# Kernel tuning notes

Measured on AMD Instinct MI355X. Metric: run time of the kernel, lower is better.

Reference implementation:

```python
import jax, jax.numpy as jnp
import numpy as np

B, G, D = 256, 64, 20          # batch, genes per term, subsystem output dim
T3, T2, T1, T0 = 2048, 512, 128, 1  # terms per stratum, deepest first
FAN = 4                        # children per internal term (root gets all T1)
EPS = 1e-5                     # BatchNorm1d eps


def setup_inputs() -> dict:
    key = jax.random.key(0)
    ks = jax.random.split(key, 32)
    def genes(k, T):
        # binary gene perturbation states (column 3 of go_gene_strata_state)
        return (jax.random.uniform(k, (B, T, G)) < 0.5).astype(jnp.float32)
    def lin(kw, kb, T, din):
        # nn.init.uniform_(w, -0.001, 0.001) per DCellSubsystem
        W = jax.random.uniform(kw, (T, din, D), minval=-0.001, maxval=0.001)
        b = jax.random.uniform(kb, (T, D), minval=-0.001, maxval=0.001)
        return W, b
    in3, in2, in1, in0 = G, FAN * D + G, FAN * D + G, T1 * D + G
    W3, b3 = lin(ks[0], ks[1], T3, in3)
    W2, b2 = lin(ks[2], ks[3], T2, in2)
    W1, b1 = lin(ks[4], ks[5], T1, in1)
    W0, b0 = lin(ks[6], ks[7], T0, in0)
    ones = lambda T: jnp.ones((T, D), jnp.float32)
    zeros = lambda T: jnp.zeros((T, D), jnp.float32)
    hw0 = jax.random.normal(ks[8], (T0, D, 1)) * 0.1
    hb0 = jnp.zeros((T0, 1), jnp.float32)
    return {
        'genes3': genes(ks[9], T3), 'genes2': genes(ks[10], T2),
        'genes1': genes(ks[11], T1), 'genes0': genes(ks[12], T0),
        'W3': W3, 'b3': b3, 'g3': ones(T3), 'be3': zeros(T3),
        'W2': W2, 'b2': b2, 'g2': ones(T2), 'be2': zeros(T2),
        'W1': W1, 'b1': b1, 'g1': ones(T1), 'be1': zeros(T1),
        'W0': W0, 'b0': b0, 'g0': ones(T0), 'be0': zeros(T0),
        'hw0': hw0, 'hb0': hb0,
    }


def _subsystem(x, W, b, g, be):
    # Linear -> BatchNorm1d (training mode, batch stats over axis 0) -> Tanh
    z = jnp.einsum('bti,tio->bto', x, W) + b          # [B, T, D]
    mu = jnp.mean(z, axis=0)
    var = jnp.var(z, axis=0)                           # biased, as in torch BN
    zn = (z - mu) * jax.lax.rsqrt(var + EPS)
    return jnp.tanh(zn * g + be)


def reference(genes3, genes2, genes1, genes0,
              W3, b3, g3, be3, W2, b2, g2, be2,
              W1, b1, g1, be1, W0, b0, g0, be0, hw0, hb0):
    # stratum 3 (leaves): input is gene states only
    h3 = _subsystem(genes3, W3, b3, g3, be3)           # [B, T3, D]
    # stratum 2: concat FAN contiguous children + own gene states
    x2 = jnp.concatenate([h3.reshape(B, T2, FAN * D), genes2], axis=-1)
    h2 = _subsystem(x2, W2, b2, g2, be2)               # [B, T2, D]
    x1 = jnp.concatenate([h2.reshape(B, T1, FAN * D), genes1], axis=-1)
    h1 = _subsystem(x1, W1, b1, g1, be1)               # [B, T1, D]
    # root: all T1 children + root gene states
    x0 = jnp.concatenate([h1.reshape(B, T0, T1 * D), genes0], axis=-1)
    h0 = _subsystem(x0, W0, b0, g0, be0)               # [B, 1, D]
    pred = jnp.einsum('bto,toc->btc', h0, hw0) + hb0   # root linear head
    return pred.reshape(B, 1)
```

## Files before the change

### kernel.cpp

```cpp
#include <hip/hip_runtime.h>
#include <hip/hip_fp16.h>


#define DEV static __device__ __forceinline__

constexpr int B_  = 256, G_ = 64, D_ = 20;
constexpr int T3_ = 2048, T2_ = 512, T1_ = 128;
constexpr float EPS_ = 1e-5f;

typedef unsigned char u8;
typedef unsigned long long u64;

constexpr size_t OFF_H2B = 0;
constexpr size_t SZ_H2 = (size_t)T2_ * B_ * D_ * 2;
constexpr size_t OFF_H1B = OFF_H2B + SZ_H2;
constexpr size_t SZ_H1 = (size_t)T1_ * B_ * D_ * 2;
constexpr size_t OFF_Z0B = OFF_H1B + SZ_H1;

typedef _Float16 half8_t __attribute__((ext_vector_type(8)));
typedef float f32x4 __attribute__((ext_vector_type(4)));

DEV half8_t as_h8(uint4 u) {
    union { uint4 u4; half8_t h; } c; c.u4 = u; return c.h;
}

DEV half8_t bits8_to_h8(uint byte) {
    uint4 r;
    r.x = ((byte & 1u)        | ((byte & 2u)   << 15)) * 0x3C00u;
    r.y = (((byte >> 2) & 1u) | ((byte & 8u)   << 13)) * 0x3C00u;
    r.z = (((byte >> 4) & 1u) | ((byte & 32u)  << 11)) * 0x3C00u;
    r.w = (((byte >> 6) & 1u) | ((byte & 128u) << 9))  * 0x3C00u;
    return as_h8(r);
}

DEV float fast_tanh(float x) {
    float e = __expf(2.0f * x);
    return fmaf(-2.0f, __builtin_amdgcn_rcpf(e + 1.0f), 1.0f);
}

__global__ __launch_bounds__(256, 2) void k_gemm32(
        const float* __restrict__ genes3, const float* __restrict__ genes2,
        const float* __restrict__ W3, const float* __restrict__ g3,
        const float* __restrict__ be3,
        const float* __restrict__ W2, const float* __restrict__ g2,
        const float* __restrict__ be2, __half* __restrict__ h2out) {
    constexpr int STRB3 = 72, STRB2 = 200;
    __shared__ __align__(16) __half h3loc[4 * B_ * D_ + 16];
    __shared__ __align__(16) __half WT3[2][32 * STRB3];
    __shared__ __align__(16) __half WT2[32 * STRB2];
    __shared__ u64 gmask[5][B_];
    __shared__ float sredb[2][4][16], qredb[2][4][16];
    __shared__ float gv3[4 * D_], bev3[4 * D_], gv2[D_], bev2[D_];

    const int t = blockIdx.x, tid = threadIdx.x;
    const int w = tid >> 6, lane = tid & 63;

    const int rb = w * 64;
#pragma unroll
    for (int s = 0; s < 5; ++s) {
        const float* gp = (s < 4)
            ? genes3 + ((size_t)rb * T3_ + 4 * t + s) * G_ + lane
            : genes2 + ((size_t)rb * T2_ + t) * G_ + lane;
        const size_t str = (size_t)(s < 4 ? T3_ : T2_) * G_;
        u64 my = 0;
#pragma unroll
        for (int r0 = 0; r0 < 64; r0 += 16) {
            float x[16];
#pragma unroll
            for (int r = 0; r < 16; ++r) x[r] = gp[(size_t)(r0 + r) * str];
#pragma unroll
            for (int r = 0; r < 16; ++r) {
                u64 m = __ballot(x[r] != 0.0f);
                if (lane == r0 + r) my = m;
            }
        }
        gmask[s][rb + lane] = my;
    }

    {
        uint* WTu = (uint*)WT2;
        for (int j = tid; j < 32 * STRB2 / 2; j += 256) WTu[j] = 0;
        if (tid < 16) h3loc[4 * B_ * D_ + tid] = __half(0.0f);
    }
    __syncthreads();

    if (tid < 4 * D_) {
        gv3[tid] = g3[(size_t)(4 * t) * D_ + tid];
        bev3[tid] = be3[(size_t)(4 * t) * D_ + tid];
    } else if (tid < 5 * D_) {
        gv2[tid - 4 * D_] = g2[(size_t)t * D_ + (tid - 4 * D_)];
        bev2[tid - 4 * D_] = be2[(size_t)t * D_ + (tid - 4 * D_)];
    }
    {
        const float* Wt = W2 + (size_t)t * (144 * D_);
        for (int j = tid; j < 144 * D_; j += 256) {
            int k_orig = j / D_, o = j - k_orig * D_;
            int k_lds;
            if (k_orig < 4 * D_) {
                int c = k_orig / D_;
                k_lds = c * 32 + (k_orig - c * D_);
            } else {
                k_lds = 4 * 32 + (k_orig - 4 * D_);
            }
            WT2[o * STRB2 + k_lds] = __float2half(Wt[j]);
        }
        const float* W3t = W3 + (size_t)(4 * t) * (G_ * D_);
#pragma unroll
        for (int i = 0; i < 5; ++i) {
            int j = tid + i * 256;
            int k = j / D_, o = j - k * D_;
            WT3[0][o * STRB3 + k] = __float2half(W3t[j]);
        }
    }
    __syncthreads();

    const int quad = lane >> 4, l15 = lane & 15;
    const int nt = w >> 1, mhalf = w & 1;
    const int ocol = nt * 16 + l15;
    const int brow_base = mhalf * 128;
    const int shq = quad * 8;
    const int oc = ocol < D_ ? ocol : D_ - 1;

#pragma unroll
    for (int c = 0; c < 4; ++c) {
        float wreg[5];
        if (c < 3) {
            const float* W3n = W3 + (size_t)(4 * t + c + 1) * (G_ * D_);
#pragma unroll
            for (int i = 0; i < 5; ++i) wreg[i] = W3n[tid + i * 256];
        }
        const __half* WTc = WT3[c & 1];
        half8_t Bf0 = as_h8(*(const uint4*)(WTc + ocol * STRB3 + quad * 8));
        half8_t Bf1 = as_h8(*(const uint4*)(WTc + ocol * STRB3 + 32 + quad * 8));

        f32x4 acc[8];
#pragma unroll
        for (int mt = 0; mt < 8; ++mt) acc[mt] = (f32x4){0.f, 0.f, 0.f, 0.f};
#pragma unroll
        for (int mt = 0; mt < 8; ++mt) {
            const int bA = brow_base + mt * 16 + l15;
            const u64 gm = gmask[c][bA];
            acc[mt] = __builtin_amdgcn_mfma_f32_16x16x32_f16(
                bits8_to_h8(((uint)gm >> shq) & 0xFFu), Bf0, acc[mt], 0, 0, 0);
            acc[mt] = __builtin_amdgcn_mfma_f32_16x16x32_f16(
                bits8_to_h8(((uint)(gm >> 32) >> shq) & 0xFFu), Bf1, acc[mt], 0, 0, 0);
        }

        if (c < 3) {
#pragma unroll
            for (int i = 0; i < 5; ++i) {
                int j = tid + i * 256;
                int k = j / D_, o = j - k * D_;
                WT3[(c + 1) & 1][o * STRB3 + k] = __float2half(wreg[i]);
            }
        }

        float s = 0.f, q = 0.f;
#pragma unroll
        for (int mt = 0; mt < 8; ++mt)
#pragma unroll
            for (int r = 0; r < 4; ++r) {
                float z = acc[mt][r];
                s += z; q += z * z;
            }
        s += __shfl_xor(s, 16, 64); q += __shfl_xor(q, 16, 64);
        s += __shfl_xor(s, 32, 64); q += __shfl_xor(q, 32, 64);
        if (lane < 16) { sredb[c & 1][w][lane] = s; qredb[c & 1][w][lane] = q; }
        __syncthreads();
        const float S = sredb[c & 1][2 * nt][l15] + sredb[c & 1][2 * nt + 1][l15];
        const float Q = qredb[c & 1][2 * nt][l15] + qredb[c & 1][2 * nt + 1][l15];
        const float mu  = S * (1.0f / B_);
        const float var = fmaxf(Q * (1.0f / B_) - mu * mu, 0.0f);
        const float rstd = rsqrtf(var + EPS_);
        const float A = rstd * gv3[c * D_ + oc];
        const float C = bev3[c * D_ + oc] - mu * A;
        if (ocol < D_) {
#pragma unroll
            for (int mt = 0; mt < 8; ++mt)
#pragma unroll
                for (int r = 0; r < 4; ++r) {
                    float h = fast_tanh(fmaf(A, acc[mt][r], C));
                    int b = brow_base + mt * 16 + quad * 4 + r;
                    h3loc[(size_t)(c * B_ + b) * D_ + ocol] = __float2half(h);
                }
        }
    }
    __syncthreads();

    half8_t Bf[6];
#pragma unroll
    for (int ks = 0; ks < 6; ++ks)
        Bf[ks] = as_h8(*(const uint4*)(WT2 + ocol * STRB2 + ks * 32 + quad * 8));

    f32x4 acc[8];
#pragma unroll
    for (int mt = 0; mt < 8; ++mt) acc[mt] = (f32x4){0.f, 0.f, 0.f, 0.f};
#pragma unroll
    for (int mt = 0; mt < 8; ++mt) {
        const int bA = brow_base + mt * 16 + l15;
        const u64 gm = gmask[4][bA];
#pragma unroll
        for (int c = 0; c < 4; ++c) {
            const __half* ap = h3loc + (size_t)(c * B_ + bA) * D_ + quad * 8;
            uint2 u0 = *(const uint2*)(ap);
            uint2 u1 = *(const uint2*)(ap + 4);
            acc[mt] = __builtin_amdgcn_mfma_f32_16x16x32_f16(
                as_h8(make_uint4(u0.x, u0.y, u1.x, u1.y)), Bf[c], acc[mt], 0, 0, 0);
        }
        acc[mt] = __builtin_amdgcn_mfma_f32_16x16x32_f16(
            bits8_to_h8(((uint)gm >> shq) & 0xFFu), Bf[4], acc[mt], 0, 0, 0);
        acc[mt] = __builtin_amdgcn_mfma_f32_16x16x32_f16(
            bits8_to_h8(((uint)(gm >> 32) >> shq) & 0xFFu), Bf[5], acc[mt], 0, 0, 0);
    }

    float s = 0.f, q = 0.f;
#pragma unroll
    for (int mt = 0; mt < 8; ++mt)
#pragma unroll
        for (int r = 0; r < 4; ++r) {
            float z = acc[mt][r];
            s += z; q += z * z;
        }
    s += __shfl_xor(s, 16, 64); q += __shfl_xor(q, 16, 64);
    s += __shfl_xor(s, 32, 64); q += __shfl_xor(q, 32, 64);
    if (lane < 16) { sredb[0][w][lane] = s; qredb[0][w][lane] = q; }
    __syncthreads();
    const float S = sredb[0][2 * nt][l15] + sredb[0][2 * nt + 1][l15];
    const float Q = qredb[0][2 * nt][l15] + qredb[0][2 * nt + 1][l15];
    const float mu  = S * (1.0f / B_);
    const float var = fmaxf(Q * (1.0f / B_) - mu * mu, 0.0f);
    const float rstd = rsqrtf(var + EPS_);
    const float A = rstd * gv2[oc];
    const float C = bev2[oc] - mu * A;

    __half* ebuf = WT2;
    if (ocol < D_) {
#pragma unroll
        for (int mt = 0; mt < 8; ++mt)
#pragma unroll
            for (int r = 0; r < 4; ++r) {
                float h = fast_tanh(fmaf(A, acc[mt][r], C));
                int b = brow_base + mt * 16 + quad * 4 + r;
                ebuf[b * D_ + ocol] = __float2half(h);
            }
    }
    __syncthreads();
    const uint4* src4 = (const uint4*)ebuf;
    uint4* dst4 = (uint4*)(h2out + (size_t)t * (B_ * D_));
    for (int j = tid; j < (B_ * D_) / 8; j += 256) dst4[j] = src4[j];
}

template <int T, int NCHILD>
__global__ __launch_bounds__(256, 4) void k_gemm(const __half* __restrict__ hsrc,
                                                 const float* __restrict__ genes,
                                                 const float* __restrict__ W,
                                                 const float* __restrict__ g,
                                                 const float* __restrict__ be,
                                                 __half* __restrict__ hout) {
    constexpr int K_IN = NCHILD * 20 + 64;
    constexpr int NK = NCHILD + 2;
    constexpr int STRB = NCHILD ? 200 : 72;
    constexpr int LDSH = (32 * STRB > B_ * D_) ? 32 * STRB : B_ * D_;
    __shared__ __align__(16) __half WT[LDSH];
    __shared__ float gv[D_], bev[D_];
    __shared__ float sred[4][16], qred[4][16];
    __shared__ u64 gmask[B_];

    const int t = blockIdx.x, tid = threadIdx.x;
    const int w = tid >> 6, lane = tid & 63;

    {
        const float* gp = genes + ((size_t)(w * 64) * T + t) * G_ + lane;
        u64 my = 0;
#pragma unroll
        for (int r0 = 0; r0 < 64; r0 += 16) {
            float x[16];
#pragma unroll
            for (int r = 0; r < 16; ++r)
                x[r] = gp[(size_t)(r0 + r) * (T * G_)];
#pragma unroll
            for (int r = 0; r < 16; ++r) {
                u64 m = __ballot(x[r] != 0.0f);
                if (lane == r0 + r) my = m;
            }
        }
        gmask[w * 64 + lane] = my;
    }

    if (NCHILD) {
        uint* WTu = (uint*)WT;
        for (int j = tid; j < 32 * STRB / 2; j += 256) WTu[j] = 0;
        __syncthreads();
    }
    if (tid < D_) { gv[tid] = g[t * D_ + tid]; bev[tid] = be[t * D_ + tid]; }
    const float* Wt = W + (size_t)t * (K_IN * D_);
    for (int j = tid; j < K_IN * D_; j += 256) {
        int k_orig = j / D_, o = j - k_orig * D_;
        int k_lds;
        if (NCHILD && k_orig < NCHILD * D_) {
            int c = k_orig / D_;
            k_lds = c * 32 + (k_orig - c * D_);
        } else {
            k_lds = NCHILD * 32 + (k_orig - NCHILD * D_);
        }
        WT[o * STRB + k_lds] = __float2half(Wt[j]);
    }
    __syncthreads();

    const int quad = lane >> 4, l15 = lane & 15;
    const int nt = w >> 1, mhalf = w & 1;
    const int ocol = nt * 16 + l15;
    const int brow_base = mhalf * 128;
    const int shq = quad * 8;

    half8_t Bf[NK];
#pragma unroll
    for (int ks = 0; ks < NK; ++ks)
        Bf[ks] = as_h8(*(const uint4*)(WT + ocol * STRB + ks * 32 + quad * 8));

    f32x4 acc[8];
#pragma unroll
    for (int mt = 0; mt < 8; ++mt) acc[mt] = (f32x4){0.f, 0.f, 0.f, 0.f};

#pragma unroll
    for (int mt = 0; mt < 8; ++mt) {
        const int bA = brow_base + mt * 16 + l15;
        const u64 gm = gmask[bA];
#pragma unroll
        for (int c = 0; c < NCHILD; ++c) {
            const __half* ap = hsrc + ((size_t)(NCHILD * t + c) * B_ + bA) * D_ + quad * 8;
            uint2 u0 = *(const uint2*)(ap);
            uint2 u1 = *(const uint2*)(ap + 4);
            acc[mt] = __builtin_amdgcn_mfma_f32_16x16x32_f16(
                as_h8(make_uint4(u0.x, u0.y, u1.x, u1.y)), Bf[c], acc[mt], 0, 0, 0);
        }
        acc[mt] = __builtin_amdgcn_mfma_f32_16x16x32_f16(
            bits8_to_h8(((uint)gm >> shq) & 0xFFu), Bf[NCHILD], acc[mt], 0, 0, 0);
        acc[mt] = __builtin_amdgcn_mfma_f32_16x16x32_f16(
            bits8_to_h8(((uint)(gm >> 32) >> shq) & 0xFFu), Bf[NCHILD + 1], acc[mt], 0, 0, 0);
    }

    float s = 0.f, q = 0.f;
#pragma unroll
    for (int mt = 0; mt < 8; ++mt)
#pragma unroll
        for (int r = 0; r < 4; ++r) {
            float z = acc[mt][r];
            s += z; q += z * z;
        }
    s += __shfl_xor(s, 16, 64); q += __shfl_xor(q, 16, 64);
    s += __shfl_xor(s, 32, 64); q += __shfl_xor(q, 32, 64);
    if (lane < 16) { sred[w][lane] = s; qred[w][lane] = q; }
    __syncthreads();
    const float S = sred[2 * nt][l15] + sred[2 * nt + 1][l15];
    const float Q = qred[2 * nt][l15] + qred[2 * nt + 1][l15];
    const float mu  = S * (1.0f / B_);
    const float var = fmaxf(Q * (1.0f / B_) - mu * mu, 0.0f);
    const float rstd = rsqrtf(var + EPS_);
    const int oc = ocol < D_ ? ocol : D_ - 1;
    const float A = rstd * gv[oc];
    const float C = bev[oc] - mu * A;

    if (ocol < D_) {
#pragma unroll
        for (int mt = 0; mt < 8; ++mt)
#pragma unroll
            for (int r = 0; r < 4; ++r) {
                float h = fast_tanh(fmaf(A, acc[mt][r], C));
                int b = brow_base + mt * 16 + quad * 4 + r;
                WT[b * D_ + ocol] = __float2half(h);
            }
    }
    __syncthreads();
    const uint4* src4 = (const uint4*)WT;
    uint4* dst4 = (uint4*)(hout + (size_t)t * (B_ * D_));
    for (int j = tid; j < (B_ * D_) / 8; j += 256) dst4[j] = src4[j];
}

__global__ __launch_bounds__(256, 4) void k_stage0a(const __half* __restrict__ h1,
                                                    const float* __restrict__ genes0,
                                                    const float* __restrict__ W0,
                                                    float* __restrict__ z0p) {
    const int b = blockIdx.x >> 2, s = blockIdx.x & 3, tid = threadIdx.x;
    const int kbase = 640 * s;
    float acc[D_] = {};
#pragma unroll
    for (int j = 0; j < 3; ++j) {
        int kl = tid + 256 * j;
        if (kl < 640) {
            int k = kbase + kl;
            int tt = k / D_, o = k - tt * D_;
            float xk = __half2float(h1[((size_t)tt * B_ + b) * D_ + o]);
            const float4* w = (const float4*)(W0 + (size_t)k * D_);
#pragma unroll
            for (int v = 0; v < D_ / 4; ++v) {
                float4 f = w[v];
                acc[4 * v + 0] = fmaf(xk, f.x, acc[4 * v + 0]);
                acc[4 * v + 1] = fmaf(xk, f.y, acc[4 * v + 1]);
                acc[4 * v + 2] = fmaf(xk, f.z, acc[4 * v + 2]);
                acc[4 * v + 3] = fmaf(xk, f.w, acc[4 * v + 3]);
            }
        }
    }
    if (s == 3 && tid < G_) {
        float xk = genes0[(size_t)b * G_ + tid];
        const float4* w = (const float4*)(W0 + (size_t)(T1_ * D_ + tid) * D_);
#pragma unroll
        for (int v = 0; v < D_ / 4; ++v) {
            float4 f = w[v];
            acc[4 * v + 0] = fmaf(xk, f.x, acc[4 * v + 0]);
            acc[4 * v + 1] = fmaf(xk, f.y, acc[4 * v + 1]);
            acc[4 * v + 2] = fmaf(xk, f.z, acc[4 * v + 2]);
            acc[4 * v + 3] = fmaf(xk, f.w, acc[4 * v + 3]);
        }
    }
    __shared__ float sred[4][D_];
    const int lane = tid & 63, wave = tid >> 6;
#pragma unroll
    for (int off = 32; off; off >>= 1)
#pragma unroll
        for (int o = 0; o < D_; ++o) acc[o] += __shfl_xor(acc[o], off, 64);
    if (lane == 0)
#pragma unroll
        for (int o = 0; o < D_; ++o) sred[wave][o] = acc[o];
    __syncthreads();
    if (tid < D_)
        z0p[((size_t)b * 4 + s) * D_ + tid] =
            sred[0][tid] + sred[1][tid] + sred[2][tid] + sred[3][tid];
}

__global__ __launch_bounds__(256) void k_stage0b(const float* __restrict__ z0p,
                                                 const float* __restrict__ g0,
                                                 const float* __restrict__ be0,
                                                 const float* __restrict__ hw0,
                                                 const float* __restrict__ hb0,
                                                 float* __restrict__ out) {
    const int tid = threadIdx.x;
    float acc[D_] = {};
#pragma unroll
    for (int s = 0; s < 4; ++s) {
        const float4* zp = (const float4*)(z0p + ((size_t)tid * 4 + s) * D_);
#pragma unroll
        for (int v = 0; v < D_ / 4; ++v) {
            float4 f = zp[v];
            acc[4 * v + 0] += f.x; acc[4 * v + 1] += f.y;
            acc[4 * v + 2] += f.z; acc[4 * v + 3] += f.w;
        }
    }
    __shared__ float sred[4][D_], qred[4][D_], Avec[D_], Cvec[D_], hwv[D_ + 1];
    const int lane = tid & 63, wave = tid >> 6;
    float s[D_], q[D_];
#pragma unroll
    for (int o = 0; o < D_; ++o) { s[o] = acc[o]; q[o] = acc[o] * acc[o]; }
#pragma unroll
    for (int off = 32; off; off >>= 1) {
#pragma unroll
        for (int o = 0; o < D_; ++o) {
            s[o] += __shfl_xor(s[o], off, 64);
            q[o] += __shfl_xor(q[o], off, 64);
        }
    }
    if (lane == 0) {
#pragma unroll
        for (int o = 0; o < D_; ++o) { sred[wave][o] = s[o]; qred[wave][o] = q[o]; }
    }
    __syncthreads();
    if (tid < D_) {
        float S = sred[0][tid] + sred[1][tid] + sred[2][tid] + sred[3][tid];
        float Q = qred[0][tid] + qred[1][tid] + qred[2][tid] + qred[3][tid];
        float mu  = S * (1.0f / B_);
        float var = fmaxf(Q * (1.0f / B_) - mu * mu, 0.0f);
        float rstd = rsqrtf(var + EPS_);
        float A = rstd * g0[tid];
        Avec[tid] = A;
        Cvec[tid] = be0[tid] - mu * A;
        hwv[tid] = hw0[tid];
    }
    if (tid == 0) hwv[D_] = hb0[0];
    __syncthreads();
    float pred = hwv[D_];
#pragma unroll
    for (int o = 0; o < D_; ++o) {
        float h = fast_tanh(fmaf(acc[o], Avec[o], Cvec[o]));
        pred = fmaf(h, hwv[o], pred);
    }
    out[tid] = pred;
}

extern "C" void kernel_launch(void* const* d_in, const int* in_sizes, int n_in,
                              void* d_out, int out_size, void* d_ws, size_t ws_size,
                              hipStream_t stream) {
    const float* genes3 = (const float*)d_in[0];
    const float* genes2 = (const float*)d_in[1];
    const float* genes1 = (const float*)d_in[2];
    const float* genes0 = (const float*)d_in[3];
    const float* W3  = (const float*)d_in[4];
    const float* g3  = (const float*)d_in[6];
    const float* be3 = (const float*)d_in[7];
    const float* W2  = (const float*)d_in[8];
    const float* g2  = (const float*)d_in[10];
    const float* be2 = (const float*)d_in[11];
    const float* W1  = (const float*)d_in[12];
    const float* g1  = (const float*)d_in[14];
    const float* be1 = (const float*)d_in[15];
    const float* W0  = (const float*)d_in[16];
    const float* g0  = (const float*)d_in[18];
    const float* be0 = (const float*)d_in[19];
    const float* hw0 = (const float*)d_in[20];
    const float* hb0 = (const float*)d_in[21];

    char* wsb = (char*)d_ws;
    __half* h2  = (__half*)(wsb + OFF_H2B);
    __half* h1  = (__half*)(wsb + OFF_H1B);
    float*  z0p = (float*)(wsb + OFF_Z0B);

    k_gemm32<<<T2_, 256, 0, stream>>>(genes3, genes2, W3, g3, be3,
                                      W2, g2, be2, h2);
    k_gemm<T1_, 4><<<T1_, 256, 0, stream>>>(h2, genes1, W1, g1, be1, h1);
    k_stage0a<<<B_ * 4, 256, 0, stream>>>(h1, genes0, W0, z0p);
    k_stage0b<<<1, 256, 0, stream>>>(z0p, g0, be0, hw0, hb0, (float*)d_out);
}
```

Measured before the change: 318.7 us.

## Prefetch next gene-mask section during MFMA and batch weight staging loads

The up-front gene bitmask construction for all five sections is replaced by building only section 0 first. Each following section's genes are loaded and ballot-packed inside the per-child loop, split around the two halves of the MFMA work, so global latency overlaps compute. Weight staging for W2, W3 and the generic stratum kernel now issues all global loads into registers before converting and scattering into LDS, which lets loads pipeline. The cost is higher register pressure (32-float buffers plus staging arrays), which could hurt occupancy under launch_bounds(256,2).

```diff
diff --git a/kernel.cpp b/kernel.cpp
--- a/kernel.cpp
+++ b/kernel.cpp
@@ -54,33 +54,33 @@
 
     const int t = blockIdx.x, tid = threadIdx.x;
     const int w = tid >> 6, lane = tid & 63;
-
     const int rb = w * 64;
-#pragma unroll
-    for (int s = 0; s < 5; ++s) {
-        const float* gp = (s < 4)
-            ? genes3 + ((size_t)rb * T3_ + 4 * t + s) * G_ + lane
-            : genes2 + ((size_t)rb * T2_ + t) * G_ + lane;
-        const size_t str = (size_t)(s < 4 ? T3_ : T2_) * G_;
-        u64 my = 0;
-#pragma unroll
-        for (int r0 = 0; r0 < 64; r0 += 16) {
-            float x[16];
-#pragma unroll
-            for (int r = 0; r < 16; ++r) x[r] = gp[(size_t)(r0 + r) * str];
-#pragma unroll
-            for (int r = 0; r < 16; ++r) {
-                u64 m = __ballot(x[r] != 0.0f);
-                if (lane == r0 + r) my = m;
-            }
-        }
-        gmask[s][rb + lane] = my;
-    }
+    const size_t str3 = (size_t)T3_ * G_;
 
     {
-        uint* WTu = (uint*)WT2;
-        for (int j = tid; j < 32 * STRB2 / 2; j += 256) WTu[j] = 0;
-        if (tid < 16) h3loc[4 * B_ * D_ + tid] = __half(0.0f);
+        const float* gp0 = genes3 + ((size_t)rb * T3_ + 4 * t) * G_ + lane;
+        float x[32];
+#pragma unroll
+        for (int r = 0; r < 32; ++r) x[r] = gp0[(size_t)r * str3];
+        {
+            uint* WTu = (uint*)WT2;
+            for (int j = tid; j < 32 * STRB2 / 2; j += 256) WTu[j] = 0;
+            if (tid < 16) h3loc[4 * B_ * D_ + tid] = __half(0.0f);
+        }
+        u64 my0 = 0;
+#pragma unroll
+        for (int r = 0; r < 32; ++r) {
+            u64 m = __ballot(x[r] != 0.0f);
+            if (lane == r) my0 = m;
+        }
+#pragma unroll
+        for (int r = 0; r < 32; ++r) x[r] = gp0[(size_t)(32 + r) * str3];
+#pragma unroll
+        for (int r = 0; r < 32; ++r) {
+            u64 m = __ballot(x[r] != 0.0f);
+            if (lane == 32 + r) my0 = m;
+        }
+        gmask[0][rb + lane] = my0;
     }
     __syncthreads();
 
@@ -92,24 +92,38 @@
         bev2[tid - 4 * D_] = be2[(size_t)t * D_ + (tid - 4 * D_)];
     }
     {
+        constexpr int NW2 = (144 * D_ + 255) / 256;
         const float* Wt = W2 + (size_t)t * (144 * D_);
-        for (int j = tid; j < 144 * D_; j += 256) {
-            int k_orig = j / D_, o = j - k_orig * D_;
-            int k_lds;
-            if (k_orig < 4 * D_) {
-                int c = k_orig / D_;
-                k_lds = c * 32 + (k_orig - c * D_);
-            } else {
-                k_lds = 4 * 32 + (k_orig - 4 * D_);
-            }
-            WT2[o * STRB2 + k_lds] = __float2half(Wt[j]);
+        float wst[NW2];
+#pragma unroll
+        for (int i = 0; i < NW2; ++i) {
+            int j = tid + i * 256;
+            wst[i] = (j < 144 * D_) ? Wt[j] : 0.0f;
         }
         const float* W3t = W3 + (size_t)(4 * t) * (G_ * D_);
+        float w3st[5];
+#pragma unroll
+        for (int i = 0; i < 5; ++i) w3st[i] = W3t[tid + i * 256];
+#pragma unroll
+        for (int i = 0; i < NW2; ++i) {
+            int j = tid + i * 256;
+            if (j < 144 * D_) {
+                int k_orig = j / D_, o = j - k_orig * D_;
+                int k_lds;
+                if (k_orig < 4 * D_) {
+                    int c = k_orig / D_;
+                    k_lds = c * 32 + (k_orig - c * D_);
+                } else {
+                    k_lds = 4 * 32 + (k_orig - 4 * D_);
+                }
+                WT2[o * STRB2 + k_lds] = __float2half(wst[i]);
+            }
+        }
 #pragma unroll
         for (int i = 0; i < 5; ++i) {
             int j = tid + i * 256;
             int k = j / D_, o = j - k * D_;
-            WT3[0][o * STRB3 + k] = __float2half(W3t[j]);
+            WT3[0][o * STRB3 + k] = __float2half(w3st[i]);
         }
     }
     __syncthreads();
@@ -123,6 +137,16 @@
 
 #pragma unroll
     for (int c = 0; c < 4; ++c) {
+        const int sec = c + 1;
+        const float* gpn = (sec < 4)
+            ? genes3 + ((size_t)rb * T3_ + 4 * t + sec) * G_ + lane
+            : genes2 + ((size_t)rb * T2_ + t) * G_ + lane;
+        const size_t strn = (sec < 4) ? str3 : (size_t)T2_ * G_;
+
+        float x[32];
+#pragma unroll
+        for (int r = 0; r < 32; ++r) x[r] = gpn[(size_t)r * strn];
+
         float wreg[5];
         if (c < 3) {
             const float* W3n = W3 + (size_t)(4 * t + c + 1) * (G_ * D_);
@@ -136,8 +160,9 @@
         f32x4 acc[8];
 #pragma unroll
         for (int mt = 0; mt < 8; ++mt) acc[mt] = (f32x4){0.f, 0.f, 0.f, 0.f};
-#pragma unroll
-        for (int mt = 0; mt < 8; ++mt) {
+
+#pragma unroll
+        for (int mt = 0; mt < 4; ++mt) {
             const int bA = brow_base + mt * 16 + l15;
             const u64 gm = gmask[c][bA];
             acc[mt] = __builtin_amdgcn_mfma_f32_16x16x32_f16(
@@ -145,6 +170,32 @@
             acc[mt] = __builtin_amdgcn_mfma_f32_16x16x32_f16(
                 bits8_to_h8(((uint)(gm >> 32) >> shq) & 0xFFu), Bf1, acc[mt], 0, 0, 0);
         }
+
+        u64 myn = 0;
+#pragma unroll
+        for (int r = 0; r < 32; ++r) {
+            u64 m = __ballot(x[r] != 0.0f);
+            if (lane == r) myn = m;
+        }
+#pragma unroll
+        for (int r = 0; r < 32; ++r) x[r] = gpn[(size_t)(32 + r) * strn];
+
+#pragma unroll
+        for (int mt = 4; mt < 8; ++mt) {
+            const int bA = brow_base + mt * 16 + l15;
+            const u64 gm = gmask[c][bA];
+            acc[mt] = __builtin_amdgcn_mfma_f32_16x16x32_f16(
+                bits8_to_h8(((uint)gm >> shq) & 0xFFu), Bf0, acc[mt], 0, 0, 0);
+            acc[mt] = __builtin_amdgcn_mfma_f32_16x16x32_f16(
+                bits8_to_h8(((uint)(gm >> 32) >> shq) & 0xFFu), Bf1, acc[mt], 0, 0, 0);
+        }
+
+#pragma unroll
+        for (int r = 0; r < 32; ++r) {
+            u64 m = __ballot(x[r] != 0.0f);
+            if (lane == 32 + r) myn = m;
+        }
+        gmask[sec][rb + lane] = myn;
 
         if (c < 3) {
 #pragma unroll
@@ -293,17 +344,30 @@
         __syncthreads();
     }
     if (tid < D_) { gv[tid] = g[t * D_ + tid]; bev[tid] = be[t * D_ + tid]; }
-    const float* Wt = W + (size_t)t * (K_IN * D_);
-    for (int j = tid; j < K_IN * D_; j += 256) {
-        int k_orig = j / D_, o = j - k_orig * D_;
-        int k_lds;
-        if (NCHILD && k_orig < NCHILD * D_) {
-            int c = k_orig / D_;
-            k_lds = c * 32 + (k_orig - c * D_);
-        } else {
-            k_lds = NCHILD * 32 + (k_orig - NCHILD * D_);
-        }
-        WT[o * STRB + k_lds] = __float2half(Wt[j]);
+    {
+        constexpr int NST = (K_IN * D_ + 255) / 256;
+        const float* Wt = W + (size_t)t * (K_IN * D_);
+        float wst[NST];
+#pragma unroll
+        for (int i = 0; i < NST; ++i) {
+            int j = tid + i * 256;
+            wst[i] = (j < K_IN * D_) ? Wt[j] : 0.0f;
+        }
+#pragma unroll
+        for (int i = 0; i < NST; ++i) {
+            int j = tid + i * 256;
+            if (j < K_IN * D_) {
+                int k_orig = j / D_, o = j - k_orig * D_;
+                int k_lds;
+                if (NCHILD && k_orig < NCHILD * D_) {
+                    int c = k_orig / D_;
+                    k_lds = c * 32 + (k_orig - c * D_);
+                } else {
+                    k_lds = NCHILD * 32 + (k_orig - NCHILD * D_);
+                }
+                WT[o * STRB + k_lds] = __float2half(wst[i]);
+            }
+        }
     }
     __syncthreads();
 
```

Result: faster. 306.0 us (-4.0%).

## Pre-pack gene states into transposed bitmasks with a coalesced pass

Applied to the files above, without the earlier changes.

Adds a kernel that reads the float gene arrays row-contiguously, ballots each row into a 64-bit mask and writes the masks transposed per term. The GEMM kernels then load one u64 per thread instead of doing strided per-batch gene reads. The weight staging loops are also split so all global loads are issued into registers before the LDS conversion stores. The cost is an extra launch, extra workspace, and a round trip of the mask data through global memory.

```diff
diff --git a/kernel.cpp b/kernel.cpp
--- a/kernel.cpp
+++ b/kernel.cpp
@@ -11,7 +11,13 @@
 typedef unsigned char u8;
 typedef unsigned long long u64;
 
-constexpr size_t OFF_H2B = 0;
+constexpr size_t OFF_GTB3 = 0;
+constexpr size_t SZ_GTB3 = (size_t)T3_ * B_ * 8;
+constexpr size_t OFF_GTB2 = OFF_GTB3 + SZ_GTB3;
+constexpr size_t SZ_GTB2 = (size_t)T2_ * B_ * 8;
+constexpr size_t OFF_GTB1 = OFF_GTB2 + SZ_GTB2;
+constexpr size_t SZ_GTB1 = (size_t)T1_ * B_ * 8;
+constexpr size_t OFF_H2B = OFF_GTB1 + SZ_GTB1;
 constexpr size_t SZ_H2 = (size_t)T2_ * B_ * D_ * 2;
 constexpr size_t OFF_H1B = OFF_H2B + SZ_H2;
 constexpr size_t SZ_H1 = (size_t)T1_ * B_ * D_ * 2;
@@ -38,8 +44,44 @@
     return fmaf(-2.0f, __builtin_amdgcn_rcpf(e + 1.0f), 1.0f);
 }
 
+__global__ __launch_bounds__(256, 8) void k_pack_all(
+        const float* __restrict__ g3s, const float* __restrict__ g2s,
+        const float* __restrict__ g1s,
+        u64* __restrict__ d3, u64* __restrict__ d2, u64* __restrict__ d1) {
+    constexpr int R3 = B_ * T3_;
+    constexpr int R2 = B_ * T2_;
+    const int lane = threadIdx.x & 63;
+    int R0 = (blockIdx.x * 4 + (threadIdx.x >> 6)) * 8;
+    const float* src; u64* dst; int shift;
+    if (R0 < R3)            { src = g3s; dst = d3; shift = 11; }
+    else if (R0 < R3 + R2)  { R0 -= R3; src = g2s; dst = d2; shift = 9; }
+    else                    { R0 -= R3 + R2; src = g1s; dst = d1; shift = 7; }
+
+    const float* p = src + (size_t)R0 * G_ + lane;
+    float x[8];
+#pragma unroll
+    for (int r = 0; r < 8; ++r) x[r] = p[r * G_];
+    u64 m[8];
+#pragma unroll
+    for (int r = 0; r < 8; ++r) m[r] = __ballot(x[r] != 0.0f);
+
+    if (lane < 8) {
+        u64 v = m[0];
+        v = lane == 1 ? m[1] : v;
+        v = lane == 2 ? m[2] : v;
+        v = lane == 3 ? m[3] : v;
+        v = lane == 4 ? m[4] : v;
+        v = lane == 5 ? m[5] : v;
+        v = lane == 6 ? m[6] : v;
+        v = lane == 7 ? m[7] : v;
+        const int R = R0 + lane;
+        const int b = R >> shift, t = R - (b << shift);
+        dst[(size_t)t * B_ + b] = v;
+    }
+}
+
 __global__ __launch_bounds__(256, 2) void k_gemm32(
-        const float* __restrict__ genes3, const float* __restrict__ genes2,
+        const u64* __restrict__ gTb3, const u64* __restrict__ gTb2,
         const float* __restrict__ W3, const float* __restrict__ g3,
         const float* __restrict__ be3,
         const float* __restrict__ W2, const float* __restrict__ g2,
@@ -55,33 +97,19 @@
     const int t = blockIdx.x, tid = threadIdx.x;
     const int w = tid >> 6, lane = tid & 63;
 
-    const int rb = w * 64;
-#pragma unroll
-    for (int s = 0; s < 5; ++s) {
-        const float* gp = (s < 4)
-            ? genes3 + ((size_t)rb * T3_ + 4 * t + s) * G_ + lane
-            : genes2 + ((size_t)rb * T2_ + t) * G_ + lane;
-        const size_t str = (size_t)(s < 4 ? T3_ : T2_) * G_;
-        u64 my = 0;
-#pragma unroll
-        for (int r0 = 0; r0 < 64; r0 += 16) {
-            float x[16];
-#pragma unroll
-            for (int r = 0; r < 16; ++r) x[r] = gp[(size_t)(r0 + r) * str];
-#pragma unroll
-            for (int r = 0; r < 16; ++r) {
-                u64 m = __ballot(x[r] != 0.0f);
-                if (lane == r0 + r) my = m;
-            }
-        }
-        gmask[s][rb + lane] = my;
-    }
+    u64 mreg[5];
+#pragma unroll
+    for (int c = 0; c < 4; ++c)
+        mreg[c] = gTb3[(size_t)(4 * t + c) * B_ + tid];
+    mreg[4] = gTb2[(size_t)t * B_ + tid];
 
     {
         uint* WTu = (uint*)WT2;
         for (int j = tid; j < 32 * STRB2 / 2; j += 256) WTu[j] = 0;
         if (tid < 16) h3loc[4 * B_ * D_ + tid] = __half(0.0f);
     }
+#pragma unroll
+    for (int s = 0; s < 5; ++s) gmask[s][tid] = mreg[s];
     __syncthreads();
 
     if (tid < 4 * D_) {
@@ -92,24 +120,38 @@
         bev2[tid - 4 * D_] = be2[(size_t)t * D_ + (tid - 4 * D_)];
     }
     {
+        constexpr int NW2 = (144 * D_ + 255) / 256;
         const float* Wt = W2 + (size_t)t * (144 * D_);
-        for (int j = tid; j < 144 * D_; j += 256) {
-            int k_orig = j / D_, o = j - k_orig * D_;
-            int k_lds;
-            if (k_orig < 4 * D_) {
-                int c = k_orig / D_;
-                k_lds = c * 32 + (k_orig - c * D_);
-            } else {
-                k_lds = 4 * 32 + (k_orig - 4 * D_);
-            }
-            WT2[o * STRB2 + k_lds] = __float2half(Wt[j]);
+        float wst[NW2];
+#pragma unroll
+        for (int i = 0; i < NW2; ++i) {
+            int j = tid + i * 256;
+            wst[i] = (j < 144 * D_) ? Wt[j] : 0.0f;
         }
         const float* W3t = W3 + (size_t)(4 * t) * (G_ * D_);
+        float w3st[5];
+#pragma unroll
+        for (int i = 0; i < 5; ++i) w3st[i] = W3t[tid + i * 256];
+#pragma unroll
+        for (int i = 0; i < NW2; ++i) {
+            int j = tid + i * 256;
+            if (j < 144 * D_) {
+                int k_orig = j / D_, o = j - k_orig * D_;
+                int k_lds;
+                if (k_orig < 4 * D_) {
+                    int c = k_orig / D_;
+                    k_lds = c * 32 + (k_orig - c * D_);
+                } else {
+                    k_lds = 4 * 32 + (k_orig - 4 * D_);
+                }
+                WT2[o * STRB2 + k_lds] = __float2half(wst[i]);
+            }
+        }
 #pragma unroll
         for (int i = 0; i < 5; ++i) {
             int j = tid + i * 256;
             int k = j / D_, o = j - k * D_;
-            WT3[0][o * STRB3 + k] = __float2half(W3t[j]);
+            WT3[0][o * STRB3 + k] = __float2half(w3st[i]);
         }
     }
     __syncthreads();
@@ -252,7 +294,7 @@
 
 template <int T, int NCHILD>
 __global__ __launch_bounds__(256, 4) void k_gemm(const __half* __restrict__ hsrc,
-                                                 const float* __restrict__ genes,
+                                                 const u64* __restrict__ gTb,
                                                  const float* __restrict__ W,
                                                  const float* __restrict__ g,
                                                  const float* __restrict__ be,
@@ -269,41 +311,40 @@
     const int t = blockIdx.x, tid = threadIdx.x;
     const int w = tid >> 6, lane = tid & 63;
 
-    {
-        const float* gp = genes + ((size_t)(w * 64) * T + t) * G_ + lane;
-        u64 my = 0;
-#pragma unroll
-        for (int r0 = 0; r0 < 64; r0 += 16) {
-            float x[16];
-#pragma unroll
-            for (int r = 0; r < 16; ++r)
-                x[r] = gp[(size_t)(r0 + r) * (T * G_)];
-#pragma unroll
-            for (int r = 0; r < 16; ++r) {
-                u64 m = __ballot(x[r] != 0.0f);
-                if (lane == r0 + r) my = m;
-            }
-        }
-        gmask[w * 64 + lane] = my;
-    }
+    const u64 mreg = gTb[(size_t)t * B_ + tid];
 
     if (NCHILD) {
         uint* WTu = (uint*)WT;
         for (int j = tid; j < 32 * STRB / 2; j += 256) WTu[j] = 0;
-        __syncthreads();
-    }
+    }
+    gmask[tid] = mreg;
+    __syncthreads();
+
     if (tid < D_) { gv[tid] = g[t * D_ + tid]; bev[tid] = be[t * D_ + tid]; }
-    const float* Wt = W + (size_t)t * (K_IN * D_);
-    for (int j = tid; j < K_IN * D_; j += 256) {
-        int k_orig = j / D_, o = j - k_orig * D_;
-        int k_lds;
-        if (NCHILD && k_orig < NCHILD * D_) {
-            int c = k_orig / D_;
-            k_lds = c * 32 + (k_orig - c * D_);
-        } else {
-            k_lds = NCHILD * 32 + (k_orig - NCHILD * D_);
-        }
-        WT[o * STRB + k_lds] = __float2half(Wt[j]);
+    {
+        constexpr int NST = (K_IN * D_ + 255) / 256;
+        const float* Wt = W + (size_t)t * (K_IN * D_);
+        float wst[NST];
+#pragma unroll
+        for (int i = 0; i < NST; ++i) {
+            int j = tid + i * 256;
+            wst[i] = (j < K_IN * D_) ? Wt[j] : 0.0f;
+        }
+#pragma unroll
+        for (int i = 0; i < NST; ++i) {
+            int j = tid + i * 256;
+            if (j < K_IN * D_) {
+                int k_orig = j / D_, o = j - k_orig * D_;
+                int k_lds;
+                if (NCHILD && k_orig < NCHILD * D_) {
+                    int c = k_orig / D_;
+                    k_lds = c * 32 + (k_orig - c * D_);
+                } else {
+                    k_lds = NCHILD * 32 + (k_orig - NCHILD * D_);
+                }
+                WT[o * STRB + k_lds] = __float2half(wst[i]);
+            }
+        }
     }
     __syncthreads();
 
@@ -510,13 +551,18 @@
     const float* hb0 = (const float*)d_in[21];
 
     char* wsb = (char*)d_ws;
+    u64* gTb3 = (u64*)(wsb + OFF_GTB3);
+    u64* gTb2 = (u64*)(wsb + OFF_GTB2);
+    u64* gTb1 = (u64*)(wsb + OFF_GTB1);
     __half* h2  = (__half*)(wsb + OFF_H2B);
     __half* h1  = (__half*)(wsb + OFF_H1B);
     float*  z0p = (float*)(wsb + OFF_Z0B);
 
-    k_gemm32<<<T2_, 256, 0, stream>>>(genes3, genes2, W3, g3, be3,
+    k_pack_all<<<688128 / 32, 256, 0, stream>>>(genes3, genes2, genes1,
+                                                gTb3, gTb2, gTb1);
+    k_gemm32<<<T2_, 256, 0, stream>>>(gTb3, gTb2, W3, g3, be3,
                                       W2, g2, be2, h2);
-    k_gemm<T1_, 4><<<T1_, 256, 0, stream>>>(h2, genes1, W1, g1, be1, h1);
+    k_gemm<T1_, 4><<<T1_, 256, 0, stream>>>(h2, gTb1, W1, g1, be1, h1);
     k_stage0a<<<B_ * 4, 256, 0, stream>>>(h1, genes0, W0, z0p);
     k_stage0b<<<1, 256, 0, stream>>>(z0p, g0, be0, hw0, hb0, (float*)d_out);
 }
```

Measured after the change: 305.1 us. 4.3% less time.
